# Performance work log

Hardware: AMD Instinct MI355X
Metric: run time of the kernel (lower is better)

## Reference

```python
import jax, jax.numpy as jnp
import numpy as np

MIN_RADIUS = 8.0  # min_radius in P2RLoss


def setup_inputs() -> dict:
    key = jax.random.key(0)
    k1, k2 = jax.random.split(key)
    B, H, W, N = 2, 160, 160, 2048
    down = 16
    dens = jax.random.normal(k1, (B, 1, H, W), dtype=jnp.float32)
    # points in full-resolution pixel coordinates [0, W*down)
    points = jax.random.uniform(k2, (B, N, 2), dtype=jnp.float32) * (W * down)
    return {"dens": dens, "points": points, "down": down}


def _bce_with_logits_weighted(logits, targets, weight):
    # mean(weight * bce_with_logits(logits, targets)), numerically stable
    elem = jnp.maximum(logits, 0.0) - logits * targets + jnp.log1p(jnp.exp(-jnp.abs(logits)))
    return jnp.mean(weight * elem)


def reference(dens, points, down):
    B, _, H, W = dens.shape
    ys, xs = jnp.meshgrid(jnp.arange(H, dtype=jnp.float32),
                          jnp.arange(W, dtype=jnp.float32), indexing='ij')
    # pixel-center coords in full resolution: [HW, 2], order (y, x)
    coords = jnp.stack([ys, xs], axis=-1).reshape(-1, 2) * down + (down - 1) / 2.0

    def per_image(den, pts):
        # den: [1, H, W]; pts: [N, 2]
        # squared L2 distances pixel->point, min over points (1-NN).
        dx = coords[:, 0, None] - pts[None, :, 0]  # [HW, N]
        dy = coords[:, 1, None] - pts[None, :, 1]  # [HW, N]
        min_d2 = jnp.min(dx * dx + dy * dy, axis=1)  # [HW]
        minC = jnp.sqrt(min_d2)  # min of sqrt == sqrt of min (monotone)
        minC = jax.lax.stop_gradient(minC)  # computed under torch.no_grad
        T = (minC < MIN_RADIUS).astype(jnp.float32).reshape(H, W, 1)
        A = den[0][..., None]  # logits, [H, W, 1] (== permute(1,2,0))
        Wt = T + 1.0
        return _bce_with_logits_weighted(A, T, Wt)

    losses = jax.vmap(per_image)(dens, points)  # [B]
    return jnp.mean(losses)  # reduction='mean' divides total by B
```

## Files before the change

### kernel.cpp

```cpp
#include <hip/hip_runtime.h>
#include <math.h>

#define B_     2
#define H_     160
#define W_     160
#define N_     2048
#define HW_    (H_ * W_)
#define BHW_   (B_ * HW_)
#define NPTS_  (B_ * N_)
#define BLOCK  256
#define TOTAL  (BHW_ + NPTS_)
#define GRID   (TOTAL / BLOCK)
#define FLAG_BYTES (BHW_ / 8)

__global__ __launch_bounds__(BLOCK) void p2r_fused_kernel(
    const float* __restrict__ dens,
    const float* __restrict__ points,
    const int*   __restrict__ down_p,
    unsigned int* __restrict__ flags,
    float*       __restrict__ out)
{
    const int tid = blockIdx.x * BLOCK + threadIdx.x;

    const float down  = (float)(*down_p);
    const float half  = (down - 1.0f) * 0.5f;
    const float scale = 1.0f / (float)(B_ * HW_);

    float v = 0.0f;

    if (tid < BHW_) {
        const float A  = dens[tid];
        const float e0 = fmaxf(A, 0.0f) + log1pf(expf(-fabsf(A)));
        v = e0 * scale;
    } else {
        const int n = tid - BHW_;
        const int b = n / N_;
        const int k = n % N_;
        const float py = points[(size_t)b * (N_ * 2) + 2 * k];
        const float px = points[(size_t)b * (N_ * 2) + 2 * k + 1];
        const int i = (int)floorf((py - half + 8.0f) / down);
        const int j = (int)floorf((px - half + 8.0f) / down);
        if (i >= 0 && i < H_ && j >= 0 && j < W_) {
            const float dy = py - ((float)i * down + half);
            const float dx = px - ((float)j * down + half);
            if (dy * dy + dx * dx < 64.0f) {
                const int pix = b * HW_ + i * W_ + j;
                const unsigned int bit = 1u << (pix & 31);
                const unsigned int old = atomicOr(&flags[pix >> 5], bit);
                if (!(old & bit)) {
                    const float A  = dens[pix];
                    const float e0 = fmaxf(A, 0.0f) + log1pf(expf(-fabsf(A)));
                    v = (e0 - 2.0f * A) * scale;
                }
            }
        }
    }

    #pragma unroll
    for (int off = 32; off > 0; off >>= 1)
        v += __shfl_down(v, off, 64);

    __shared__ float sred[BLOCK / 64];
    const int wave = threadIdx.x >> 6;
    if ((threadIdx.x & 63) == 0) sred[wave] = v;
    __syncthreads();
    if (threadIdx.x == 0)
        atomicAdd(out, sred[0] + sred[1] + sred[2] + sred[3]);
}

extern "C" void kernel_launch(void* const* d_in, const int* in_sizes, int n_in,
                              void* d_out, int out_size, void* d_ws, size_t ws_size,
                              hipStream_t stream) {
    const float* dens   = (const float*)d_in[0];
    const float* points = (const float*)d_in[1];
    const int*   down   = (const int*)d_in[2];
    float*       out    = (float*)d_out;
    unsigned int* flags = (unsigned int*)d_ws;

    hipMemsetAsync(flags, 0, FLAG_BYTES, stream);
    hipMemsetAsync(out, 0, sizeof(float), stream);

    p2r_fused_kernel<<<GRID, BLOCK, 0, stream>>>(dens, points, down, flags, out);
}
```

Baseline: 61.90 us.

## Collapse loss into single-block kernel with shared-memory flags, dropping memsets

Replaces the multi-block kernel and its two preceding memset launches with one 1024-thread block. The dedup bitmask now lives in LDS, zeroed in-kernel, and the final sum is written directly instead of atomically accumulated. Dense BCE terms are processed with float4 loads in a strided loop. This removes per-launch and memset overhead, at the cost of running all the transcendental and memory work on a single CU.

```diff
diff --git a/kernel.cpp b/kernel.cpp
--- a/kernel.cpp
+++ b/kernel.cpp
@@ -8,38 +8,38 @@
 #define HW_    (H_ * W_)
 #define BHW_   (B_ * HW_)
 #define NPTS_  (B_ * N_)
-#define BLOCK  256
-#define TOTAL  (BHW_ + NPTS_)
-#define GRID   (TOTAL / BLOCK)
-#define FLAG_BYTES (BHW_ / 8)
+#define BLOCK  1024
+#define NWAVE  (BLOCK / 64)
+#define FLAG_WORDS (BHW_ / 32)
 
-__global__ __launch_bounds__(BLOCK) void p2r_fused_kernel(
+__global__ __launch_bounds__(BLOCK) void p2r_single_kernel(
     const float* __restrict__ dens,
     const float* __restrict__ points,
     const int*   __restrict__ down_p,
-    unsigned int* __restrict__ flags,
     float*       __restrict__ out)
 {
-    const int tid = blockIdx.x * BLOCK + threadIdx.x;
+    __shared__ unsigned int flags[FLAG_WORDS];
+    __shared__ float sred[NWAVE];
+
+    const int tid = threadIdx.x;
 
     const float down  = (float)(*down_p);
     const float half  = (down - 1.0f) * 0.5f;
     const float scale = 1.0f / (float)(B_ * HW_);
 
+    for (int w = tid; w < FLAG_WORDS; w += BLOCK)
+        flags[w] = 0u;
+    __syncthreads();
+
     float v = 0.0f;
 
-    if (tid < BHW_) {
-        const float A  = dens[tid];
-        const float e0 = fmaxf(A, 0.0f) + log1pf(expf(-fabsf(A)));
-        v = e0 * scale;
-    } else {
-        const int n = tid - BHW_;
+    for (int n = tid; n < NPTS_; n += BLOCK) {
         const int b = n / N_;
-        const int k = n % N_;
+        const int k = n - b * N_;
         const float py = points[(size_t)b * (N_ * 2) + 2 * k];
         const float px = points[(size_t)b * (N_ * 2) + 2 * k + 1];
-        const int i = (int)floorf((py - half + 8.0f) / down);
-        const int j = (int)floorf((px - half + 8.0f) / down);
+        const int i = (int)floorf((py - half) / down + 0.5f);
+        const int j = (int)floorf((px - half) / down + 0.5f);
         if (i >= 0 && i < H_ && j >= 0 && j < W_) {
             const float dy = py - ((float)i * down + half);
             const float dx = px - ((float)j * down + half);
@@ -50,22 +50,34 @@
                 if (!(old & bit)) {
                     const float A  = dens[pix];
                     const float e0 = fmaxf(A, 0.0f) + log1pf(expf(-fabsf(A)));
-                    v = (e0 - 2.0f * A) * scale;
+                    v += (e0 - 2.0f * A) * scale;
                 }
             }
         }
     }
 
+    const float4* __restrict__ dens4 = (const float4*)dens;
+    for (int q = tid; q < BHW_ / 4; q += BLOCK) {
+        const float4 a = dens4[q];
+        float e;
+        e  = fmaxf(a.x, 0.0f) + log1pf(expf(-fabsf(a.x)));
+        e += fmaxf(a.y, 0.0f) + log1pf(expf(-fabsf(a.y)));
+        e += fmaxf(a.z, 0.0f) + log1pf(expf(-fabsf(a.z)));
+        e += fmaxf(a.w, 0.0f) + log1pf(expf(-fabsf(a.w)));
+        v += e * scale;
+    }
+
     #pragma unroll
     for (int off = 32; off > 0; off >>= 1)
         v += __shfl_down(v, off, 64);
-
-    __shared__ float sred[BLOCK / 64];
-    const int wave = threadIdx.x >> 6;
-    if ((threadIdx.x & 63) == 0) sred[wave] = v;
+    if ((tid & 63) == 0) sred[tid >> 6] = v;
     __syncthreads();
-    if (threadIdx.x == 0)
-        atomicAdd(out, sred[0] + sred[1] + sred[2] + sred[3]);
+    if (tid == 0) {
+        float total = 0.0f;
+        #pragma unroll
+        for (int w = 0; w < NWAVE; ++w) total += sred[w];
+        out[0] = total;
+    }
 }
 
 extern "C" void kernel_launch(void* const* d_in, const int* in_sizes, int n_in,
@@ -75,10 +87,6 @@
     const float* points = (const float*)d_in[1];
     const int*   down   = (const int*)d_in[2];
     float*       out    = (float*)d_out;
-    unsigned int* flags = (unsigned int*)d_ws;
 
-    hipMemsetAsync(flags, 0, FLAG_BYTES, stream);
-    hipMemsetAsync(out, 0, sizeof(float), stream);
-
-    p2r_fused_kernel<<<GRID, BLOCK, 0, stream>>>(dens, points, down, flags, out);
+    p2r_single_kernel<<<1, BLOCK, 0, stream>>>(dens, points, down, out);
 }
```

Result: slower. 97.34 us (+57.3%).
